# Kernel tuning notes

Hardware: AMD Instinct MI355X
Metric: run time of the kernel (lower is better)

## Reference

```python
import jax, jax.numpy as jnp
import numpy as np

EPS = 1e-5

def group_points(feat, idx):
    # feat: [B, C, N1], idx: [B, N2, K] -> [B, C, N2, K]
    return jax.vmap(lambda f, i: f[:, i])(feat, idx)

def conv_bn_relu(x, W, gamma, beta):
    # 1x1 conv2d (no bias) + training-mode BatchNorm2d + ReLU
    y = jnp.einsum('oc,bcnk->bonk', W, x)
    mean = y.mean(axis=(0, 2, 3), keepdims=True)
    var = y.var(axis=(0, 2, 3), keepdims=True)  # biased, as BN uses for normalization
    y = (y - mean) * jax.lax.rsqrt(var + EPS)
    y = y * gamma[None, :, None, None] + beta[None, :, None, None]
    return jax.nn.relu(y)

def setup_inputs() -> dict:
    key = jax.random.key(0)
    ks = jax.random.split(key, 12)
    B, N1, N2, K, C1 = 16, 4096, 1024, 32, 64
    mlp = [C1 + 3, 64, 64, 128]  # use_xyz adds 3 channels
    inp = {
        'in_xyz': jax.random.normal(ks[0], (B, 3, N1), jnp.float32),
        'out_xyz': jax.random.normal(ks[1], (B, 3, N2), jnp.float32),
        'in_feature': jax.random.normal(ks[2], (B, C1, N1), jnp.float32),
        'nbr_index': jax.random.randint(ks[3], (B, N2, K), 0, N1, jnp.int32),
    }
    for li in range(3):
        cin, cout = mlp[li], mlp[li + 1]
        inp[f'W{li}'] = jax.random.normal(ks[4 + li], (cout, cin), jnp.float32) * (1.0 / np.sqrt(cin))
        inp[f'g{li}'] = jnp.ones((cout,), jnp.float32)
        inp[f'b{li}'] = jnp.zeros((cout,), jnp.float32)
    return inp

def reference(in_xyz, out_xyz, in_feature, nbr_index,
              W0, g0, b0, W1, g1, b1, W2, g2, b2):
    # gather neighbor features: [B, C1, N2, K]
    nbr_feature = group_points(in_feature, nbr_index)
    # gather neighbor xyz, recenter on query points: [B, 3, N2, K]
    nbr_xyz = group_points(in_xyz, nbr_index) - out_xyz[:, :, :, None]
    x = jnp.concatenate([nbr_feature, nbr_xyz], axis=1)  # [B, C1+3, N2, K]
    x = conv_bn_relu(x, W0, g0, b0)
    x = conv_bn_relu(x, W1, g1, b1)
    x = conv_bn_relu(x, W2, g2, b2)
    return jnp.max(x, axis=3)  # [B, C2, N2]
```

## Files before the change

### kernel.cpp

```cpp
#include <hip/hip_runtime.h>
#include <cstdint>

typedef unsigned short u16;
typedef unsigned int   u32;
typedef __attribute__((ext_vector_type(8))) short  short8;
typedef __attribute__((ext_vector_type(4))) float  floatx4;

#define NPTS 524288
#define NREP 4

__device__ __forceinline__ float b2f(u16 h) { return __uint_as_float(((u32)h) << 16); }
__device__ __forceinline__ u16 f2b(float f) {
  u32 u = __float_as_uint(f);
  return (u16)((u + 0x7FFFu + ((u >> 16) & 1u)) >> 16);
}
__device__ __forceinline__ u32 pk_bf16(float lo, float hi) {
  return (u32)f2b(lo) | ((u32)f2b(hi) << 16);
}
__device__ __forceinline__ short8 ld_frag8(const u16* p) {
  union { uint4 q; short8 s; } x;
  x.q = *(const uint4*)p;
  return x.s;
}
__device__ __forceinline__ short8 u4_to_s8(uint4 q) {
  union { uint4 q; short8 s; } x; x.q = q; return x.s;
}

__global__ __launch_bounds__(256) void prep_all(const float* __restrict__ inf,
                                                const float* __restrict__ ixyz,
                                                const float* __restrict__ W0,
                                                const float* __restrict__ W1,
                                                const float* __restrict__ W2,
                                                u16* __restrict__ featT,
                                                float4* __restrict__ xyzT,
                                                u16* __restrict__ Wb,
                                                float* __restrict__ gz) {
  __shared__ float tile[32 * 33];
  const int bk = blockIdx.x, t = threadIdx.x;
  if (bk < 4096) {
    int b = bk >> 8, rem = bk & 255, cc = rem >> 7, nc = rem & 127;
    #pragma unroll
    for (int i = 0; i < 4; ++i) {
      int flat = t + i * 256;
      int cl = flat >> 5, nl = flat & 31;
      tile[cl * 33 + nl] = inf[(size_t)((b * 64) + cc * 32 + cl) * 4096 + nc * 32 + nl];
    }
    __syncthreads();
    #pragma unroll
    for (int i = 0; i < 4; ++i) {
      int flat = t + i * 256;
      int nl = flat >> 5, cl = flat & 31;
      featT[(size_t)((b << 12) + nc * 32 + nl) * 64 + cc * 32 + cl] = f2b(tile[cl * 33 + nl]);
    }
  } else if (bk < 4352) {
    int g = (bk - 4096) * 256 + t;
    int b = g >> 12, n = g & 4095;
    const float* p = ixyz + (size_t)b * 12288;
    xyzT[g] = make_float4(p[n], p[4096 + n], p[8192 + n], 0.f);
  } else if (bk < 4432) {
    int s = (bk - 4352) * 256 + t;
    u16 v = 0;
    if (s < 6656)       { int o = s / 104, c = s % 104; if (c < 67) v = f2b(W0[o * 67 + c]); }
    else if (s < 11264) { int q = s - 6656;  int o = q / 72, c = q % 72; if (c < 64) v = f2b(W1[o * 64 + c]); }
    else                { int q = s - 11264; int o = q / 72, c = q % 72; if (c < 64) v = f2b(W2[o * 64 + c]); }
    Wb[s] = v;
  } else {
    #pragma unroll
    for (int i = 0; i < 8; ++i) gz[t + i * 256] = 0.f;
  }
}

template<int KSTEPS, int OCH, bool GATHER, bool MAXOUT>
__global__ __launch_bounds__(256, MAXOUT ? 4 : 5) void gemm_layer(
    const u16* __restrict__ xsrc, const float4* __restrict__ xyzT,
    const float* __restrict__ oxyz, const int* __restrict__ nbr,
    const u16* __restrict__ Wb,
    const float* __restrict__ gsin, const float* __restrict__ gam,
    const float* __restrict__ bet,
    u16* __restrict__ yout, u32* __restrict__ gm,
    float* __restrict__ gsout) {
  constexpr int PITCH = KSTEPS * 32 + 8;
  __shared__ __align__(16) u16 wsh[OCH * PITCH];
  __shared__ float red[512];
  __shared__ float ss[GATHER ? 4 : 128];

  const int t = threadIdx.x, blk = blockIdx.x;
  const int lane = t & 63, wv = t >> 6, lr = lane & 15, quad = lane >> 4;
  const int P0 = blk * 256;
  const int b = blk >> 7;

  {
    const u32* src = (const u32*)Wb;
    u32* dst = (u32*)wsh;
    constexpr int NW = OCH * PITCH / 2;
    #pragma unroll
    for (int i = 0; i < NW / 256; ++i) dst[t + i * 256] = src[t + i * 256];
  }
  if constexpr (!GATHER) {
    if (t < 64) {
      float a = 0.f, q = 0.f;
      #pragma unroll
      for (int rep = 0; rep < NREP; ++rep) {
        a += gsin[rep * 128 + t];
        q += gsin[rep * 128 + 64 + t];
      }
      const float invN = 1.f / (float)NPTS;
      float mean = a * invN;
      float var  = fmaxf(q * invN - mean * mean, 0.f);
      float sc = gam[t] * rsqrtf(var + 1e-5f);
      ss[t] = sc; ss[64 + t] = bet[t] - mean * sc;
    }
  }
  __syncthreads();

  float scr[2][8], shr[2][8];
  if constexpr (!GATHER) {
    #pragma unroll
    for (int ks = 0; ks < 2; ++ks)
      #pragma unroll
      for (int i = 0; i < 8; ++i) {
        const int c = ks * 32 + quad * 8 + i;
        scr[ks][i] = ss[c]; shr[ks][i] = ss[64 + c];
      }
  }

  float s1[4] = {0.f, 0.f, 0.f, 0.f}, s2[4] = {0.f, 0.f, 0.f, 0.f};
  u32* yo = (u32*)yout;

  if constexpr (!MAXOUT) {
    const u16* bp = wsh + lr * PITCH + quad * 8;
    #pragma unroll
    for (int sub = 0; sub < 4; ++sub) {
      const int R = P0 + sub * 64 + wv * 16 + lr;
      short8 av[KSTEPS];
      if constexpr (GATHER) {
        const int id = nbr[R];
        const u16* row = xsrc + (size_t)((b << 12) + id) * 64;
        uint4 a0 = *(const uint4*)(row + quad * 8);
        uint4 a1 = *(const uint4*)(row + quad * 8 + 32);
        u32 w0 = 0u, w1 = 0u;
        if (quad == 0) {
          const int n2 = (R & 32767) >> 5;
          float4 p = xyzT[(b << 12) + id];
          float dx = p.x - oxyz[(b * 3 + 0) * 1024 + n2];
          float dy = p.y - oxyz[(b * 3 + 1) * 1024 + n2];
          float dz = p.z - oxyz[(b * 3 + 2) * 1024 + n2];
          w0 = pk_bf16(dx, dy); w1 = (u32)f2b(dz);
        }
        av[0] = u4_to_s8(a0);
        av[1] = u4_to_s8(a1);
        av[2] = u4_to_s8(make_uint4(w0, w1, 0u, 0u));
      } else {
        const u16* row = xsrc + ((size_t)R << 6);
        #pragma unroll
        for (int ks = 0; ks < KSTEPS; ++ks) {
          uint4 raw = *(const uint4*)(row + ks * 32 + quad * 8);
          u32 w[4] = { raw.x, raw.y, raw.z, raw.w };
          u32 o[4];
          #pragma unroll
          for (int j = 0; j < 4; ++j) {
            float lo = fmaxf(b2f((u16)(w[j] & 0xffffu)) * scr[ks][2 * j]     + shr[ks][2 * j],     0.f);
            float hi = fmaxf(b2f((u16)(w[j] >> 16))     * scr[ks][2 * j + 1] + shr[ks][2 * j + 1], 0.f);
            o[j] = pk_bf16(lo, hi);
          }
          av[ks] = u4_to_s8(make_uint4(o[0], o[1], o[2], o[3]));
        }
      }
      floatx4 acc[4];
      #pragma unroll
      for (int nt = 0; nt < 4; ++nt) acc[nt] = (floatx4){0.f, 0.f, 0.f, 0.f};
      #pragma unroll
      for (int ks = 0; ks < KSTEPS; ++ks)
        #pragma unroll
        for (int nt = 0; nt < 4; ++nt) {
          short8 bv = ld_frag8(bp + nt * 16 * PITCH + ks * 32);
          acc[nt] = __builtin_amdgcn_mfma_f32_16x16x32_bf16(av[ks], bv, acc[nt], 0, 0, 0);
        }
      const int R0 = P0 + sub * 64 + wv * 16 + quad * 4;
      #pragma unroll
      for (int nt = 0; nt < 4; ++nt)
        #pragma unroll
        for (int r = 0; r < 4; ++r) {
          float v = acc[nt][r];
          s1[nt] += v; s2[nt] += v * v;
          float vo = __shfl_xor(v, 1);
          if ((lr & 1) == 0)
            yo[(size_t)(R0 + r) * 32 + nt * 8 + (lr >> 1)] = pk_bf16(v, vo);
        }
    }
  } else {
    const int rg = wv >> 1, cg = wv & 1;
    const u16* bp = wsh + (cg * 64 + lr) * PITCH + quad * 8;
    for (int sub = 0; sub < 4; ++sub) {
      short8 av[2][2];
      #pragma unroll
      for (int h = 0; h < 2; ++h) {
        const int R = P0 + sub * 64 + rg * 32 + h * 16 + lr;
        const u16* row = xsrc + ((size_t)R << 6);
        #pragma unroll
        for (int ks = 0; ks < 2; ++ks) {
          uint4 raw = *(const uint4*)(row + ks * 32 + quad * 8);
          u32 w[4] = { raw.x, raw.y, raw.z, raw.w };
          u32 o[4];
          #pragma unroll
          for (int j = 0; j < 4; ++j) {
            float lo = fmaxf(b2f((u16)(w[j] & 0xffffu)) * scr[ks][2 * j]     + shr[ks][2 * j],     0.f);
            float hi = fmaxf(b2f((u16)(w[j] >> 16))     * scr[ks][2 * j + 1] + shr[ks][2 * j + 1], 0.f);
            o[j] = pk_bf16(lo, hi);
          }
          av[h][ks] = u4_to_s8(make_uint4(o[0], o[1], o[2], o[3]));
        }
      }
      floatx4 acc[2][4];
      #pragma unroll
      for (int h = 0; h < 2; ++h)
        #pragma unroll
        for (int nt = 0; nt < 4; ++nt) acc[h][nt] = (floatx4){0.f, 0.f, 0.f, 0.f};
      #pragma unroll
      for (int ks = 0; ks < 2; ++ks)
        #pragma unroll
        for (int nt = 0; nt < 4; ++nt) {
          short8 bv = ld_frag8(bp + nt * 16 * PITCH + ks * 32);
          #pragma unroll
          for (int h = 0; h < 2; ++h)
            acc[h][nt] = __builtin_amdgcn_mfma_f32_16x16x32_bf16(av[h][ks], bv, acc[h][nt], 0, 0, 0);
        }
      float mx[4], mn[4];
      #pragma unroll
      for (int nt = 0; nt < 4; ++nt) {
        mx[nt] = -INFINITY; mn[nt] = INFINITY;
        #pragma unroll
        for (int h = 0; h < 2; ++h)
          #pragma unroll
          for (int r = 0; r < 4; ++r) {
            float v = acc[h][nt][r];
            s1[nt] += v; s2[nt] += v * v;
            mx[nt] = fmaxf(mx[nt], v); mn[nt] = fminf(mn[nt], v);
          }
        mx[nt] = fmaxf(mx[nt], __shfl_xor(mx[nt], 16));
        mx[nt] = fmaxf(mx[nt], __shfl_xor(mx[nt], 32));
        mn[nt] = fminf(mn[nt], __shfl_xor(mn[nt], 16));
        mn[nt] = fminf(mn[nt], __shfl_xor(mn[nt], 32));
      }
      if (lane < 16) {
        const int grp = blk * 8 + sub * 2 + rg;
        #pragma unroll
        for (int nt = 0; nt < 4; ++nt)
          gm[(size_t)grp * 128 + cg * 64 + nt * 16 + lr] = pk_bf16(mx[nt], mn[nt]);
      }
    }
  }

  #pragma unroll
  for (int nt = 0; nt < 4; ++nt) {
    s1[nt] += __shfl_xor(s1[nt], 16); s1[nt] += __shfl_xor(s1[nt], 32);
    s2[nt] += __shfl_xor(s2[nt], 16); s2[nt] += __shfl_xor(s2[nt], 32);
  }
  if (lane < 16) {
    #pragma unroll
    for (int nt = 0; nt < 4; ++nt) {
      red[wv * 64 + nt * 16 + lr] = s1[nt];
      red[256 + wv * 64 + nt * 16 + lr] = s2[nt];
    }
  }
  __syncthreads();
  float* gb = gsout + (blk & (NREP - 1)) * (MAXOUT ? 256 : 128);
  if constexpr (!MAXOUT) {
    if (t < 64) {
      unsafeAtomicAdd(&gb[t], red[t] + red[64 + t] + red[128 + t] + red[192 + t]);
    } else if (t < 128) {
      int c = t - 64;
      unsafeAtomicAdd(&gb[64 + c], red[256 + c] + red[320 + c] + red[384 + c] + red[448 + c]);
    }
  } else {
    if (t < 128) {
      int half = t >> 6, i = t & 63;
      unsafeAtomicAdd(&gb[t], red[half * 64 + i] + red[(half + 2) * 64 + i]);
    } else {
      int c = t - 128, half = c >> 6, i = c & 63;
      unsafeAtomicAdd(&gb[128 + c], red[256 + half * 64 + i] + red[256 + (half + 2) * 64 + i]);
    }
  }
}

__global__ __launch_bounds__(256) void final_out(const u32* __restrict__ gm,
                                                 const float* __restrict__ gs,
                                                 const float* __restrict__ gam,
                                                 const float* __restrict__ bet,
                                                 float* __restrict__ out) {
  __shared__ float tile[64 * 33];
  __shared__ float ssc[128], ssh[128];
  int blk = blockIdx.x;
  int b = blk >> 6, rem = blk & 63, cc = rem >> 4, nn = rem & 15;
  int t = threadIdx.x;
  if (t < 128) {
    float a = 0.f, q = 0.f;
    #pragma unroll
    for (int rep = 0; rep < NREP; ++rep) {
      a += gs[rep * 256 + t];
      q += gs[rep * 256 + 128 + t];
    }
    const float invN = 1.f / (float)NPTS;
    float mean = a * invN;
    float var  = fmaxf(q * invN - mean * mean, 0.f);
    float sc = gam[t] * rsqrtf(var + 1e-5f);
    ssc[t] = sc; ssh[t] = bet[t] - mean * sc;
  }
  __syncthreads();
  #pragma unroll
  for (int i = 0; i < 8; ++i) {
    int flat = t + i * 256;
    int n2l = flat >> 5, cl = flat & 31;
    int c = cc * 32 + cl;
    size_t idx = (size_t)((b << 10) + nn * 64 + n2l) * 128 + c;
    u32 p = gm[idx];
    float mxv = b2f((u16)(p & 0xffffu)), mnv = b2f((u16)(p >> 16));
    float scv = ssc[c], shv = ssh[c];
    float v = (scv >= 0.f) ? mxv : mnv;
    tile[n2l * 33 + cl] = fmaxf(scv * v + shv, 0.f);
  }
  __syncthreads();
  #pragma unroll
  for (int i = 0; i < 8; ++i) {
    int flat = t + i * 256;
    int cl = flat >> 6, n2l = flat & 63;
    out[(size_t)((b * 128) + cc * 32 + cl) * 1024 + nn * 64 + n2l] = tile[n2l * 33 + cl];
  }
}

extern "C" void kernel_launch(void* const* d_in, const int* in_sizes, int n_in,
                              void* d_out, int out_size, void* d_ws, size_t ws_size,
                              hipStream_t stream) {
  const float* in_xyz  = (const float*)d_in[0];
  const float* out_xyz = (const float*)d_in[1];
  const float* in_feat = (const float*)d_in[2];
  const int*   nbr     = (const int*)d_in[3];
  const float* W0 = (const float*)d_in[4];
  const float* g0 = (const float*)d_in[5];
  const float* b0 = (const float*)d_in[6];
  const float* W1 = (const float*)d_in[7];
  const float* g1 = (const float*)d_in[8];
  const float* b1 = (const float*)d_in[9];
  const float* W2 = (const float*)d_in[10];
  const float* g2 = (const float*)d_in[11];
  const float* b2 = (const float*)d_in[12];
  float* out = (float*)d_out;

  char* ws = (char*)d_ws;
  u16*    Wb    = (u16*)(ws + 4096);
  float*  gs0   = (float*)(ws + 49152);
  float*  gs1   = (float*)(ws + 51200);
  float*  gs2   = (float*)(ws + 53248);
  u16*    featT = (u16*)(ws + 262144);
  float4* xyzT  = (float4*)(ws + 8650752);
  u16*    y0    = (u16*)(ws + 9699328);
  u16*    y1    = (u16*)(ws + 76808192);
  u32*    gm    = (u32*)(ws + 9699328);

  hipLaunchKernelGGL(prep_all, dim3(4433), dim3(256), 0, stream,
                     in_feat, in_xyz, W0, W1, W2, featT, xyzT, Wb, gs0);

  hipLaunchKernelGGL((gemm_layer<3, 64, true, false>), dim3(2048), dim3(256), 0, stream,
                     featT, xyzT, out_xyz, nbr, Wb, nullptr, nullptr, nullptr,
                     y0, nullptr, gs0);

  hipLaunchKernelGGL((gemm_layer<2, 64, false, false>), dim3(2048), dim3(256), 0, stream,
                     y0, nullptr, nullptr, nullptr, Wb + 6656, gs0, g0, b0,
                     y1, nullptr, gs1);

  hipLaunchKernelGGL((gemm_layer<2, 128, false, true>), dim3(2048), dim3(256), 0, stream,
                     y1, nullptr, nullptr, nullptr, Wb + 11264, gs1, g1, b1,
                     nullptr, gm, gs2);

  hipLaunchKernelGGL(final_out, dim3(1024), dim3(256), 0, stream, gm, gs2, g2, b2, out);
}
```

Measured before the change: 226.8 us.

## Fold query-point recentering into per-block correction and use nontemporal loads/stores

Stores neighbor xyz as packed bf16 (8 bytes per point instead of a float4) and drops the per-row subtraction of the query xyz in the gather. The offset is instead applied algebraically after the MFMA, as a precomputed W0[:,64:67]·out_xyz correction held in shared memory per query point. It also switches the streaming activation loads, index loads and y0 stores to nontemporal hints to reduce cache pollution. The trade-off is a numerics change: absolute xyz is rounded to bf16 before the subtraction rather than the difference, which can lose precision.

New measurement: 294.7 us. 30.0% more time.

```diff
diff --git a/kernel.cpp b/kernel.cpp
--- a/kernel.cpp
+++ b/kernel.cpp
@@ -5,6 +5,7 @@
 typedef unsigned int   u32;
 typedef __attribute__((ext_vector_type(8))) short  short8;
 typedef __attribute__((ext_vector_type(4))) float  floatx4;
+typedef __attribute__((ext_vector_type(4))) unsigned int u32x4;
 
 #define NPTS 524288
 #define NREP 4
@@ -24,6 +25,9 @@
 }
 __device__ __forceinline__ short8 u4_to_s8(uint4 q) {
   union { uint4 q; short8 s; } x; x.q = q; return x.s;
+}
+__device__ __forceinline__ u32x4 nt_ld4(const void* p) {
+  return __builtin_nontemporal_load((const u32x4*)p);
 }
 
 __global__ __launch_bounds__(256) void prep_all(const float* __restrict__ inf,
@@ -32,7 +36,7 @@
                                                 const float* __restrict__ W1,
                                                 const float* __restrict__ W2,
                                                 u16* __restrict__ featT,
-                                                float4* __restrict__ xyzT,
+                                                u16* __restrict__ xyzB,
                                                 u16* __restrict__ Wb,
                                                 float* __restrict__ gz) {
   __shared__ float tile[32 * 33];
@@ -56,7 +60,9 @@
     int g = (bk - 4096) * 256 + t;
     int b = g >> 12, n = g & 4095;
     const float* p = ixyz + (size_t)b * 12288;
-    xyzT[g] = make_float4(p[n], p[4096 + n], p[8192 + n], 0.f);
+    u32 lo = pk_bf16(p[n], p[4096 + n]);
+    u32 hi = (u32)f2b(p[8192 + n]);
+    *(uint2*)(xyzB + (size_t)g * 4) = make_uint2(lo, hi);
   } else if (bk < 4432) {
     int s = (bk - 4352) * 256 + t;
     u16 v = 0;
@@ -72,7 +78,7 @@
 
 template<int KSTEPS, int OCH, bool GATHER, bool MAXOUT>
 __global__ __launch_bounds__(256, MAXOUT ? 4 : 5) void gemm_layer(
-    const u16* __restrict__ xsrc, const float4* __restrict__ xyzT,
+    const u16* __restrict__ xsrc, const u16* __restrict__ xyzB,
     const float* __restrict__ oxyz, const int* __restrict__ nbr,
     const u16* __restrict__ Wb,
     const float* __restrict__ gsin, const float* __restrict__ gam,
@@ -83,6 +89,7 @@
   __shared__ __align__(16) u16 wsh[OCH * PITCH];
   __shared__ float red[512];
   __shared__ float ss[GATHER ? 4 : 128];
+  __shared__ float corr[GATHER ? 8 : 1][64];
 
   const int t = threadIdx.x, blk = blockIdx.x;
   const int lane = t & 63, wv = t >> 6, lr = lane & 15, quad = lane >> 4;
@@ -96,7 +103,18 @@
     #pragma unroll
     for (int i = 0; i < NW / 256; ++i) dst[t + i * 256] = src[t + i * 256];
   }
-  if constexpr (!GATHER) {
+  if constexpr (GATHER) {
+    #pragma unroll
+    for (int half = 0; half < 2; ++half) {
+      int e = t + half * 256, nn = e >> 6, och = e & 63;
+      int n2 = (blk * 8 + nn) & 1023;
+      float c = 0.f;
+      #pragma unroll
+      for (int k = 0; k < 3; ++k)
+        c += b2f(Wb[och * 104 + 64 + k]) * oxyz[((b * 3 + k) << 10) + n2];
+      corr[nn][och] = c;
+    }
+  } else {
     if (t < 64) {
       float a = 0.f, q = 0.f;
       #pragma unroll
@@ -134,18 +152,14 @@
       const int R = P0 + sub * 64 + wv * 16 + lr;
       short8 av[KSTEPS];
       if constexpr (GATHER) {
-        const int id = nbr[R];
+        const int id = __builtin_nontemporal_load(&nbr[R]);
         const u16* row = xsrc + (size_t)((b << 12) + id) * 64;
         uint4 a0 = *(const uint4*)(row + quad * 8);
         uint4 a1 = *(const uint4*)(row + quad * 8 + 32);
         u32 w0 = 0u, w1 = 0u;
         if (quad == 0) {
-          const int n2 = (R & 32767) >> 5;
-          float4 p = xyzT[(b << 12) + id];
-          float dx = p.x - oxyz[(b * 3 + 0) * 1024 + n2];
-          float dy = p.y - oxyz[(b * 3 + 1) * 1024 + n2];
-          float dz = p.z - oxyz[(b * 3 + 2) * 1024 + n2];
-          w0 = pk_bf16(dx, dy); w1 = (u32)f2b(dz);
+          uint2 v = *(const uint2*)(xyzB + (size_t)((b << 12) + id) * 4);
+          w0 = v.x; w1 = v.y;
         }
         av[0] = u4_to_s8(a0);
         av[1] = u4_to_s8(a1);
@@ -154,8 +168,8 @@
         const u16* row = xsrc + ((size_t)R << 6);
         #pragma unroll
         for (int ks = 0; ks < KSTEPS; ++ks) {
-          uint4 raw = *(const uint4*)(row + ks * 32 + quad * 8);
-          u32 w[4] = { raw.x, raw.y, raw.z, raw.w };
+          u32x4 raw = nt_ld4(row + ks * 32 + quad * 8);
+          u32 w[4] = { raw[0], raw[1], raw[2], raw[3] };
           u32 o[4];
           #pragma unroll
           for (int j = 0; j < 4; ++j) {
@@ -177,15 +191,22 @@
           acc[nt] = __builtin_amdgcn_mfma_f32_16x16x32_bf16(av[ks], bv, acc[nt], 0, 0, 0);
         }
       const int R0 = P0 + sub * 64 + wv * 16 + quad * 4;
+      float corrv[4] = {0.f, 0.f, 0.f, 0.f};
+      if constexpr (GATHER) {
+        const int nn = sub * 2 + (wv >> 1);
+        #pragma unroll
+        for (int nt = 0; nt < 4; ++nt) corrv[nt] = corr[nn][nt * 16 + lr];
+      }
       #pragma unroll
       for (int nt = 0; nt < 4; ++nt)
         #pragma unroll
         for (int r = 0; r < 4; ++r) {
-          float v = acc[nt][r];
+          float v = acc[nt][r] - corrv[nt];
           s1[nt] += v; s2[nt] += v * v;
           float vo = __shfl_xor(v, 1);
           if ((lr & 1) == 0)
-            yo[(size_t)(R0 + r) * 32 + nt * 8 + (lr >> 1)] = pk_bf16(v, vo);
+            __builtin_nontemporal_store(pk_bf16(v, vo),
+                &yo[(size_t)(R0 + r) * 32 + nt * 8 + (lr >> 1)]);
         }
     }
   } else {
@@ -199,8 +220,8 @@
         const u16* row = xsrc + ((size_t)R << 6);
         #pragma unroll
         for (int ks = 0; ks < 2; ++ks) {
-          uint4 raw = *(const uint4*)(row + ks * 32 + quad * 8);
-          u32 w[4] = { raw.x, raw.y, raw.z, raw.w };
+          u32x4 raw = nt_ld4(row + ks * 32 + quad * 8);
+          u32 w[4] = { raw[0], raw[1], raw[2], raw[3] };
           u32 o[4];
           #pragma unroll
           for (int j = 0; j < 4; ++j) {
@@ -352,16 +373,16 @@
   float*  gs1   = (float*)(ws + 51200);
   float*  gs2   = (float*)(ws + 53248);
   u16*    featT = (u16*)(ws + 262144);
-  float4* xyzT  = (float4*)(ws + 8650752);
+  u16*    xyzB  = (u16*)(ws + 8650752);
   u16*    y0    = (u16*)(ws + 9699328);
   u16*    y1    = (u16*)(ws + 76808192);
   u32*    gm    = (u32*)(ws + 9699328);
 
   hipLaunchKernelGGL(prep_all, dim3(4433), dim3(256), 0, stream,
-                     in_feat, in_xyz, W0, W1, W2, featT, xyzT, Wb, gs0);
+                     in_feat, in_xyz, W0, W1, W2, featT, xyzB, Wb, gs0);
 
   hipLaunchKernelGGL((gemm_layer<3, 64, true, false>), dim3(2048), dim3(256), 0, stream,
-                     featT, xyzT, out_xyz, nbr, Wb, nullptr, nullptr, nullptr,
+                     featT, xyzB, out_xyz, nbr, Wb, nullptr, nullptr, nullptr,
                      y0, nullptr, gs0);
 
   hipLaunchKernelGGL((gemm_layer<2, 64, false, false>), dim3(2048), dim3(256), 0, stream,
```
